# Optimization experiments

Hardware: AMD Instinct MI355X
Metric: run time of the kernel (lower is better)

## Reference

```python
import jax, jax.numpy as jnp
import numpy as np
from jax import lax

IN_FEATURES = 8192
OUT_FEATURES = 28672


def _unpack3(qweight, infeatures):
    """Unpack GPTQ-style 3-bit weights.

    qweight: (infeatures//32*3, O) int32. Every 3 consecutive int32 rows hold
    32 packed 3-bit values per column (GPTQ quant.py packing): values 0-9 in
    word0 bits [0..30), value 10 split over word0[30:32]|word1[0:1],
    values 11-20 in word1 bits [1..31), value 21 split over word1[31:32]|word2[0:2],
    values 22-31 in word2 bits [2..32).
    Returns float32 (infeatures, O) with raw quant codes in [0, 8).
    """
    O = qweight.shape[1]
    G = infeatures // 32
    q = lax.bitcast_convert_type(qweight, jnp.uint32).reshape(G, 3, O)
    w0, w1, w2 = q[:, 0], q[:, 1], q[:, 2]
    sh = jnp.arange(10, dtype=jnp.uint32)  # 10 whole values per word
    v0 = (w0[:, None, :] >> (3 * sh)[None, :, None]) & 7          # (G,10,O)
    v10 = (((w0 >> 30) & 3) | ((w1 & 1) << 2))[:, None, :]        # (G,1,O)
    v1 = (w1[:, None, :] >> (3 * sh + 1)[None, :, None]) & 7       # (G,10,O)
    v21 = (((w1 >> 31) & 1) | ((w2 & 3) << 1))[:, None, :]        # (G,1,O)
    v2 = (w2[:, None, :] >> (3 * sh + 2)[None, :, None]) & 7       # (G,10,O)
    vals = jnp.concatenate([v0, v10, v1, v21, v2], axis=1)        # (G,32,O)
    return vals.reshape(infeatures, O).astype(jnp.float32)


def setup_inputs() -> dict:
    key = jax.random.key(0)
    k1, k2, k3, k4, k5 = jax.random.split(key, 5)
    x = jax.random.normal(k1, (1, IN_FEATURES), dtype=jnp.float32)
    qweight = jax.random.randint(k2, (IN_FEATURES // 32 * 3, OUT_FEATURES), 0, 2147483647, dtype=jnp.int32)
    scales = jax.random.uniform(k3, (OUT_FEATURES, 1), dtype=jnp.float32)
    zeros = jax.random.normal(k4, (OUT_FEATURES, 1), dtype=jnp.float32)
    bias = jax.random.normal(k5, (OUT_FEATURES,), dtype=jnp.float32)
    return {"x": x, "qweight": qweight, "scales": scales, "zeros": zeros, "bias": bias}


def reference(x, qweight, scales, zeros, bias):
    infeatures = x.shape[-1]
    q = _unpack3(qweight, infeatures)            # (K, O) float codes
    # per-output-channel dequant: W[k, o] = scales[o] * q[k, o] - zeros[o]
    W = scales.T * q - zeros.T                   # (K, O)
    y = x @ W + bias                             # (1, O)
    return y
```

## Files before the change

### kernel.cpp

```cpp
#include <hip/hip_runtime.h>
#include <stdint.h>


constexpr int O_FEAT  = 28672;
constexpr int IN_FEAT = 8192;
constexpr int NGROUP  = IN_FEAT / 32;
constexpr int SPLIT   = 32;
constexpr int GPB     = NGROUP / SPLIT;
constexpr int O4      = O_FEAT / 4;

__device__ __forceinline__ void dot_group(uint32_t w0, uint32_t w1, uint32_t w2,
                                          const float xv[32], float& acc) {
  float a0 = acc, a1 = 0.f, a2 = 0.f;
  #pragma unroll
  for (int j = 0; j < 10; ++j) a0 += xv[j] * (float)((w0 >> (3 * j)) & 7u);
  a0 += xv[10] * (float)((w0 >> 30) | ((w1 & 1u) << 2));
  #pragma unroll
  for (int j = 0; j < 10; ++j) a1 += xv[11 + j] * (float)((w1 >> (3 * j + 1)) & 7u);
  a1 += xv[21] * (float)((w1 >> 31) | ((w2 & 3u) << 1));
  #pragma unroll
  for (int j = 0; j < 10; ++j) a2 += xv[22 + j] * (float)((w2 >> (3 * j + 2)) & 7u);
  acc = a0 + (a1 + a2);
}

__global__ __launch_bounds__(256) void q3_partial(const float* __restrict__ x,
                                                  const uint4* __restrict__ qw4,
                                                  float* __restrict__ part) {
  const int tcol4 = blockIdx.x * 256 + threadIdx.x;
  const int g0    = blockIdx.y * GPB;
  const uint4* qp = qw4 + (size_t)(3 * g0) * O4 + tcol4;

  __shared__ float xs[GPB * 32];
  xs[threadIdx.x] = x[g0 * 32 + threadIdx.x];
  __syncthreads();

  float acc0 = 0.f, acc1 = 0.f, acc2 = 0.f, acc3 = 0.f;

  uint4 na = qp[0], nb = qp[O4], nc = qp[2 * O4];
  for (int g = 0; g < GPB; ++g) {
    const uint4 wa = na, wb = nb, wc = nc;
    qp += (g < GPB - 1) ? 3 * O4 : 0;
    na = qp[0]; nb = qp[O4]; nc = qp[2 * O4];

    float xv[32];
    const float4* s4 = reinterpret_cast<const float4*>(&xs[g * 32]);
    #pragma unroll
    for (int u = 0; u < 8; ++u) {
      float4 t = s4[u];
      xv[4 * u + 0] = t.x; xv[4 * u + 1] = t.y;
      xv[4 * u + 2] = t.z; xv[4 * u + 3] = t.w;
    }

    dot_group(wa.x, wb.x, wc.x, xv, acc0);
    dot_group(wa.y, wb.y, wc.y, xv, acc1);
    dot_group(wa.z, wb.z, wc.z, xv, acc2);
    dot_group(wa.w, wb.w, wc.w, xv, acc3);
  }

  float4 r = make_float4(acc0, acc1, acc2, acc3);
  reinterpret_cast<float4*>(part)[(size_t)blockIdx.y * O4 + tcol4] = r;
}

__global__ __launch_bounds__(256) void q3_finish(const float* __restrict__ x,
                                                 const float* __restrict__ part,
                                                 const float* __restrict__ scales,
                                                 const float* __restrict__ zeros,
                                                 const float* __restrict__ bias,
                                                 float* __restrict__ out) {
  float s = 0.f;
  const float4* x4 = reinterpret_cast<const float4*>(x);
  for (int i = threadIdx.x; i < IN_FEAT / 4; i += 256) {
    float4 t = x4[i];
    s += (t.x + t.y) + (t.z + t.w);
  }
  #pragma unroll
  for (int off = 32; off > 0; off >>= 1) s += __shfl_down(s, off, 64);
  __shared__ float ls[4];
  if ((threadIdx.x & 63) == 0) ls[threadIdx.x >> 6] = s;
  __syncthreads();
  float S = (ls[0] + ls[1]) + (ls[2] + ls[3]);

  int o = blockIdx.x * 256 + threadIdx.x;
  float s0 = 0.f, s1 = 0.f, s2 = 0.f, s3 = 0.f;
  #pragma unroll
  for (int y = 0; y < SPLIT; y += 4) {
    s0 += part[(size_t)(y + 0) * O_FEAT + o];
    s1 += part[(size_t)(y + 1) * O_FEAT + o];
    s2 += part[(size_t)(y + 2) * O_FEAT + o];
    s3 += part[(size_t)(y + 3) * O_FEAT + o];
  }
  float sum = (s0 + s1) + (s2 + s3);
  out[o] = scales[o] * sum - zeros[o] * S + bias[o];
}

extern "C" void kernel_launch(void* const* d_in, const int* in_sizes, int n_in,
                              void* d_out, int out_size, void* d_ws, size_t ws_size,
                              hipStream_t stream) {
  const float* x      = (const float*)d_in[0];
  const uint4* qw4    = (const uint4*)d_in[1];
  const float* scales = (const float*)d_in[2];
  const float* zeros  = (const float*)d_in[3];
  const float* bias   = (const float*)d_in[4];
  float*       out    = (float*)d_out;
  float*       part   = (float*)d_ws;

  q3_partial<<<dim3(O_FEAT / (256 * 4), SPLIT), dim3(256), 0, stream>>>(x, qw4, part);
  q3_finish<<<dim3(O_FEAT / 256), dim3(256), 0, stream>>>(x, part, scales, zeros, bias, out);
}
```

Before: 145.5 us.

## Use packed float2 FMAs in dequant dot and split finish reduction

Rewrites the 3-bit dot product to pair adjacent codes into two-wide float vectors so the compiler can emit packed FP32 FMAs (v_pk_fma_f32), roughly halving the FMA instruction count. The partial kernel also computes per-split sums of x into a small workspace. The finish kernel then reads those instead of re-reducing all of x in every block, and it splits the 32-way partial reduction across four wavefronts with more blocks. The cost is extra int-to-float conversions packed into vectors and a shared-memory reduction step; the main kernel is likely still bound by memory bandwidth.

```diff
diff --git a/kernel.cpp b/kernel.cpp
--- a/kernel.cpp
+++ b/kernel.cpp
@@ -1,6 +1,8 @@
 #include <hip/hip_runtime.h>
 #include <stdint.h>
 
+
+typedef float v2f __attribute__((ext_vector_type(2)));
 
 constexpr int O_FEAT  = 28672;
 constexpr int IN_FEAT = 8192;
@@ -9,32 +11,56 @@
 constexpr int GPB     = NGROUP / SPLIT;
 constexpr int O4      = O_FEAT / 4;
 
-__device__ __forceinline__ void dot_group(uint32_t w0, uint32_t w1, uint32_t w2,
-                                          const float xv[32], float& acc) {
-  float a0 = acc, a1 = 0.f, a2 = 0.f;
+__device__ __forceinline__ void dot_group_pk(uint32_t w0, uint32_t w1, uint32_t w2,
+                                             const v2f xv[16], v2f& acc) {
+  v2f a0 = acc, a1 = {0.f, 0.f};
   #pragma unroll
-  for (int j = 0; j < 10; ++j) a0 += xv[j] * (float)((w0 >> (3 * j)) & 7u);
-  a0 += xv[10] * (float)((w0 >> 30) | ((w1 & 1u) << 2));
+  for (int t = 0; t < 5; ++t) {
+    v2f q = { (float)((w0 >> (6 * t)) & 7u), (float)((w0 >> (6 * t + 3)) & 7u) };
+    (t & 1 ? a1 : a0) += xv[t] * q;
+  }
+  {
+    v2f q = { (float)((w0 >> 30) | ((w1 & 1u) << 2)), (float)((w1 >> 1) & 7u) };
+    a1 += xv[5] * q;
+  }
   #pragma unroll
-  for (int j = 0; j < 10; ++j) a1 += xv[11 + j] * (float)((w1 >> (3 * j + 1)) & 7u);
-  a1 += xv[21] * (float)((w1 >> 31) | ((w2 & 3u) << 1));
+  for (int t = 0; t < 4; ++t) {
+    v2f q = { (float)((w1 >> (4 + 6 * t)) & 7u), (float)((w1 >> (7 + 6 * t)) & 7u) };
+    (t & 1 ? a1 : a0) += xv[6 + t] * q;
+  }
+  {
+    v2f q = { (float)((w1 >> 28) & 7u), (float)((w1 >> 31) | ((w2 & 3u) << 1)) };
+    a0 += xv[10] * q;
+  }
   #pragma unroll
-  for (int j = 0; j < 10; ++j) a2 += xv[22 + j] * (float)((w2 >> (3 * j + 2)) & 7u);
-  acc = a0 + (a1 + a2);
+  for (int t = 0; t < 5; ++t) {
+    v2f q = { (float)((w2 >> (2 + 6 * t)) & 7u), (float)((w2 >> (5 + 6 * t)) & 7u) };
+    (t & 1 ? a1 : a0) += xv[11 + t] * q;
+  }
+  acc = a0 + a1;
 }
 
 __global__ __launch_bounds__(256) void q3_partial(const float* __restrict__ x,
                                                   const uint4* __restrict__ qw4,
-                                                  float* __restrict__ part) {
+                                                  float* __restrict__ part,
+                                                  float* __restrict__ partS) {
   const int tcol4 = blockIdx.x * 256 + threadIdx.x;
   const int g0    = blockIdx.y * GPB;
   const uint4* qp = qw4 + (size_t)(3 * g0) * O4 + tcol4;
 
   __shared__ float xs[GPB * 32];
-  xs[threadIdx.x] = x[g0 * 32 + threadIdx.x];
+  const float myx = x[g0 * 32 + threadIdx.x];
+  xs[threadIdx.x] = myx;
+
+  float s = myx;
+  #pragma unroll
+  for (int off = 32; off > 0; off >>= 1) s += __shfl_down(s, off, 64);
+  __shared__ float ls[4];
+  if ((threadIdx.x & 63) == 0) ls[threadIdx.x >> 6] = s;
   __syncthreads();
+  if (threadIdx.x == 0) partS[blockIdx.y] = (ls[0] + ls[1]) + (ls[2] + ls[3]);
 
-  float acc0 = 0.f, acc1 = 0.f, acc2 = 0.f, acc3 = 0.f;
+  v2f acc0 = {0.f, 0.f}, acc1 = {0.f, 0.f}, acc2 = {0.f, 0.f}, acc3 = {0.f, 0.f};
 
   uint4 na = qp[0], nb = qp[O4], nc = qp[2 * O4];
   for (int g = 0; g < GPB; ++g) {
@@ -42,55 +68,56 @@
     qp += (g < GPB - 1) ? 3 * O4 : 0;
     na = qp[0]; nb = qp[O4]; nc = qp[2 * O4];
 
-    float xv[32];
+    v2f xv[16];
     const float4* s4 = reinterpret_cast<const float4*>(&xs[g * 32]);
     #pragma unroll
     for (int u = 0; u < 8; ++u) {
       float4 t = s4[u];
-      xv[4 * u + 0] = t.x; xv[4 * u + 1] = t.y;
-      xv[4 * u + 2] = t.z; xv[4 * u + 3] = t.w;
+      xv[2 * u]     = v2f{t.x, t.y};
+      xv[2 * u + 1] = v2f{t.z, t.w};
     }
 
-    dot_group(wa.x, wb.x, wc.x, xv, acc0);
-    dot_group(wa.y, wb.y, wc.y, xv, acc1);
-    dot_group(wa.z, wb.z, wc.z, xv, acc2);
-    dot_group(wa.w, wb.w, wc.w, xv, acc3);
+    dot_group_pk(wa.x, wb.x, wc.x, xv, acc0);
+    dot_group_pk(wa.y, wb.y, wc.y, xv, acc1);
+    dot_group_pk(wa.z, wb.z, wc.z, xv, acc2);
+    dot_group_pk(wa.w, wb.w, wc.w, xv, acc3);
   }
 
-  float4 r = make_float4(acc0, acc1, acc2, acc3);
+  float4 r = make_float4(acc0.x + acc0.y, acc1.x + acc1.y,
+                         acc2.x + acc2.y, acc3.x + acc3.y);
   reinterpret_cast<float4*>(part)[(size_t)blockIdx.y * O4 + tcol4] = r;
 }
 
-__global__ __launch_bounds__(256) void q3_finish(const float* __restrict__ x,
-                                                 const float* __restrict__ part,
+__global__ __launch_bounds__(256) void q3_finish(const float* __restrict__ part,
+                                                 const float* __restrict__ partS,
                                                  const float* __restrict__ scales,
                                                  const float* __restrict__ zeros,
                                                  const float* __restrict__ bias,
                                                  float* __restrict__ out) {
-  float s = 0.f;
-  const float4* x4 = reinterpret_cast<const float4*>(x);
-  for (int i = threadIdx.x; i < IN_FEAT / 4; i += 256) {
-    float4 t = x4[i];
-    s += (t.x + t.y) + (t.z + t.w);
+  const int q  = threadIdx.x >> 6;
+  const int ol = threadIdx.x & 63;
+  const int o  = blockIdx.x * 64 + ol;
+
+  float S = 0.f;
+  #pragma unroll
+  for (int i = 0; i < 8; ++i) {
+    float4 t = reinterpret_cast<const float4*>(partS)[i];
+    S += (t.x + t.y) + (t.z + t.w);
   }
+
+  float s0 = 0.f, s1 = 0.f;
   #pragma unroll
-  for (int off = 32; off > 0; off >>= 1) s += __shfl_down(s, off, 64);
-  __shared__ float ls[4];
-  if ((threadIdx.x & 63) == 0) ls[threadIdx.x >> 6] = s;
+  for (int y = 0; y < 8; y += 2) {
+    s0 += part[(size_t)(8 * q + y)     * O_FEAT + o];
+    s1 += part[(size_t)(8 * q + y + 1) * O_FEAT + o];
+  }
+  __shared__ float red[4][64];
+  red[q][ol] = s0 + s1;
   __syncthreads();
-  float S = (ls[0] + ls[1]) + (ls[2] + ls[3]);
-
-  int o = blockIdx.x * 256 + threadIdx.x;
-  float s0 = 0.f, s1 = 0.f, s2 = 0.f, s3 = 0.f;
-  #pragma unroll
-  for (int y = 0; y < SPLIT; y += 4) {
-    s0 += part[(size_t)(y + 0) * O_FEAT + o];
-    s1 += part[(size_t)(y + 1) * O_FEAT + o];
-    s2 += part[(size_t)(y + 2) * O_FEAT + o];
-    s3 += part[(size_t)(y + 3) * O_FEAT + o];
+  if (q == 0) {
+    float tot = (red[0][ol] + red[1][ol]) + (red[2][ol] + red[3][ol]);
+    out[o] = scales[o] * tot - zeros[o] * S + bias[o];
   }
-  float sum = (s0 + s1) + (s2 + s3);
-  out[o] = scales[o] * sum - zeros[o] * S + bias[o];
 }
 
 extern "C" void kernel_launch(void* const* d_in, const int* in_sizes, int n_in,
@@ -103,7 +130,8 @@
   const float* bias   = (const float*)d_in[4];
   float*       out    = (float*)d_out;
   float*       part   = (float*)d_ws;
+  float*       partS  = (float*)d_ws + (size_t)SPLIT * O_FEAT;
 
-  q3_partial<<<dim3(O_FEAT / (256 * 4), SPLIT), dim3(256), 0, stream>>>(x, qw4, part);
-  q3_finish<<<dim3(O_FEAT / 256), dim3(256), 0, stream>>>(x, part, scales, zeros, bias, out);
+  q3_partial<<<dim3(O_FEAT / (256 * 4), SPLIT), dim3(256), 0, stream>>>(x, qw4, part, partS);
+  q3_finish<<<dim3(O_FEAT / 64), dim3(256), 0, stream>>>(part, partS, scales, zeros, bias, out);
 }
```

New measurement: 142.6 us. 2.0% less time.
